# Kernel optimization log

Measured on AMD Instinct MI355X. Metric: run time of the kernel, lower is better.

The kernel has to match this reference:

```python
import jax, jax.numpy as jnp
import numpy as np

K = 3        # kernel_size
PAD = 1      # padding
STRIDE = 1   # stride (must be 1: module asserts offset HxW == input HxW)
DIL = 1      # dilation


def _bilinear_gather(x, py, px):
    """x: (B,C,H,W); py,px: (B,KK,Ho,Wo) float sample coords.
    Returns (B,C,KK,Ho,Wo), zero outside bounds (DCNv2 semantics)."""
    B, C, H, W = x.shape
    y0 = jnp.floor(py); x0 = jnp.floor(px)
    wy1 = py - y0; wy0 = 1.0 - wy1
    wx1 = px - x0; wx0 = 1.0 - wx1
    flat = x.reshape(B, C, H * W)

    def gather(yi, xi):
        valid = (yi >= 0) & (yi < H) & (xi >= 0) & (xi < W)
        yc = jnp.clip(yi, 0, H - 1).astype(jnp.int32)
        xc = jnp.clip(xi, 0, W - 1).astype(jnp.int32)
        idx = (yc * W + xc).reshape(B, 1, -1)                      # (B,1,KK*Ho*Wo)
        g = jnp.take_along_axis(flat, jnp.broadcast_to(idx, (B, C, idx.shape[-1])), axis=2)
        g = g.reshape(B, C, *yi.shape[1:])                          # (B,C,KK,Ho,Wo)
        return jnp.where(valid[:, None], g, 0.0)

    v00 = gather(y0, x0)
    v01 = gather(y0, x0 + 1)
    v10 = gather(y0 + 1, x0)
    v11 = gather(y0 + 1, x0 + 1)
    wy0 = wy0[:, None]; wy1 = wy1[:, None]; wx0 = wx0[:, None]; wx1 = wx1[:, None]
    return wy0 * (wx0 * v00 + wx1 * v01) + wy1 * (wx0 * v10 + wx1 * v11)


def dcn_v2(x, coord_offset, coord_weight, weight, bias):
    B, C, H, W = x.shape
    O = weight.shape[0]
    KK = K * K
    # offset channels ordered (k, [y,x]) per DCNv2 layout
    offs = coord_offset.reshape(B, KK, 2, H, W)
    oy, ox = offs[:, :, 0], offs[:, :, 1]
    ky, kx = jnp.meshgrid(jnp.arange(K), jnp.arange(K), indexing='ij')
    ky = ky.reshape(KK); kx = kx.reshape(KK)
    # base sampling grid for each output pixel / kernel tap: (KK,H,W)
    py = (jnp.arange(H) * STRIDE - PAD)[None, :, None] + (ky * DIL)[:, None, None]
    px = (jnp.arange(W) * STRIDE - PAD)[None, None, :] + (kx * DIL)[:, None, None]
    py = py.astype(x.dtype)[None] + oy   # (B,KK,H,W)
    px = px.astype(x.dtype)[None] + ox
    sampled = _bilinear_gather(x, py, px)              # (B,C,KK,H,W)
    sampled = sampled * coord_weight[:, None]          # modulation mask
    out = jnp.einsum('bckhw,ock->bohw', sampled, weight.reshape(O, C, KK))
    return out + bias[None, :, None, None]


def setup_inputs() -> dict:
    key = jax.random.key(0)
    k1, k2, k3, k4, k5 = jax.random.split(key, 5)
    B, C, O, H, W = 8, 256, 256, 64, 64
    return {
        'input': jax.random.normal(k1, (B, C, H, W), dtype=jnp.float32),
        'coord_offset': jax.random.normal(k2, (B, 2 * K * K, H, W), dtype=jnp.float32),
        'coord_weight': jax.random.uniform(k3, (B, K * K, H, W), dtype=jnp.float32),
        'weight': jax.random.normal(k4, (O, C, K, K), dtype=jnp.float32) * 0.02,
        'bias': jax.random.normal(k5, (O,), dtype=jnp.float32) * 0.01,
    }


def reference(input, coord_offset, coord_weight, weight, bias):
    return dcn_v2(input, coord_offset, coord_weight, weight, bias)
```

## Files before the change

kernel.cpp:

```cpp
#include <hip/hip_runtime.h>
#include <hip/hip_bf16.h>
#include <stdint.h>

typedef _Float16 f16_t;
typedef f16_t f16x8 __attribute__((ext_vector_type(8)));
typedef f16_t f16x2 __attribute__((ext_vector_type(2)));
typedef float f32x4 __attribute__((ext_vector_type(4)));

__device__ inline f16x2 as_f16x2(int v) {
    union { int i; f16x2 h; } u; u.i = v; return u.h;
}

__global__ __launch_bounds__(256) void k_prep(const float* __restrict__ x,
                                              const float* __restrict__ w,
                                              f16_t* __restrict__ xt,
                                              f16_t* __restrict__ Wp) {
    __shared__ __align__(16) char smem[36864];
    const int t = threadIdx.x;
    if (blockIdx.x < 512) {
        f16_t (*tT)[264] = (f16_t(*)[264])smem;
        const int b = blockIdx.x >> 6;
        const int y = blockIdx.x & 63;
        const float* src = x + ((size_t)(b * 256) * 64 + y) * 64;
        const int x4 = (t & 15) * 4;
        const int cs = t >> 4;
#pragma unroll
        for (int cc = 0; cc < 256; cc += 16) {
            int c = cc + cs;
            float4 v = *(const float4*)(src + (size_t)c * 4096 + x4);
            tT[x4 + 0][c] = (f16_t)v.x;
            tT[x4 + 1][c] = (f16_t)v.y;
            tT[x4 + 2][c] = (f16_t)v.z;
            tT[x4 + 3][c] = (f16_t)v.w;
        }
        __syncthreads();
        f16_t* dst = xt + ((size_t)(b * 64 + y) * 64) * 256;
#pragma unroll
        for (int i = 0; i < 8; ++i) {
            const int s = t + 256 * i;
            const int xx = s >> 5, cg = s & 31;
            *(f16x8*)(dst + xx * 256 + cg * 8) = *(const f16x8*)&tT[xx][cg * 8];
        }
    } else {
        float* lw = (float*)smem;
        const int o0 = (blockIdx.x - 512) * 4;
        const float4* src = (const float4*)(w + (size_t)o0 * 2304);
#pragma unroll
        for (int i = 0; i < 9; ++i)
            ((float4*)lw)[t + 256 * i] = src[t + 256 * i];
        __syncthreads();
#pragma unroll
        for (int i = 0; i < 5; ++i) {
            const int u = t + 256 * i;
            if (u < 1152) {
                const int o = u / 288, r = u - o * 288;
                const int kb2 = r >> 3, rr = r & 7;
                const int s = rr >> 2, qq = rr & 3;
                const int kk = kb2 >> 2, cp = kb2 & 3;
                f16x8 v;
#pragma unroll
                for (int e = 0; e < 8; ++e) {
                    const int c = cp * 64 + s * 32 + qq * 8 + e;
                    v[e] = (f16_t)lw[o * 2304 + c * 9 + kk];
                }
                *(f16x8*)(Wp + ((size_t)(kb2 * 2 + s) * 256 + o0 + o) * 32 + qq * 8) = v;
            }
        }
    }
}

__global__ __launch_bounds__(512, 4) void k_dcn(
    const f16_t* __restrict__ xt, const f16_t* __restrict__ Wp,
    const float* __restrict__ coff, const float* __restrict__ cwm,
    const float* __restrict__ bias, float* __restrict__ out) {

    __shared__ __align__(16) f16_t sS[2][64 * 64];
    __shared__ __align__(16) int2 sT[9 * 64 * 4];

    const int blk = blockIdx.x;
    const int b  = blk & 7;
    const int h  = blk >> 3;
    const int t = threadIdx.x;
    const int wv = t >> 6;
    const int lane = t & 63;

    const int p = t >> 3;
    const int q = t & 7;

    const int fr = lane & 15;
    const int quad = lane >> 4;
    const int swz = fr & 7;

    for (int u = t; u < 576; u += 512) {
        const int kk = u >> 6, wpx = u & 63;
        float oy = coff[((size_t)(b * 18 + kk * 2 + 0) * 64 + h) * 64 + wpx];
        float ox = coff[((size_t)(b * 18 + kk * 2 + 1) * 64 + h) * 64 + wpx];
        float m  = cwm [((size_t)(b * 9 + kk) * 64 + h) * 64 + wpx];
        float py = (float)(h - 1 + (kk / 3)) + oy;
        float px = (float)(wpx - 1 + (kk % 3)) + ox;
        float fy = floorf(py), fx = floorf(px);
        int y0 = (int)fy, x0 = (int)fx;
        int y1 = y0 + 1,  x1 = x0 + 1;
        float wy1 = py - fy, wx1 = px - fx;
        float wy0 = 1.0f - wy1, wx0 = 1.0f - wx1;
        bool vy0 = (y0 >= 0) && (y0 < 64), vy1 = (y1 >= 0) && (y1 < 64);
        bool vx0 = (x0 >= 0) && (x0 < 64), vx1 = (x1 >= 0) && (x1 < 64);
        int yc0 = min(max(y0, 0), 63), yc1 = min(max(y1, 0), 63);
        int xc0 = min(max(x0, 0), 63), xc1 = min(max(x1, 0), 63);
        const int base = b * 4096;
        float cw[4];
        int   ca[4];
        cw[0] = (vy0 && vx0) ? wy0 * wx0 * m : 0.0f;
        cw[1] = (vy0 && vx1) ? wy0 * wx1 * m : 0.0f;
        cw[2] = (vy1 && vx0) ? wy1 * wx0 * m : 0.0f;
        cw[3] = (vy1 && vx1) ? wy1 * wx1 * m : 0.0f;
        ca[0] = (base + yc0 * 64 + xc0) * 512;
        ca[1] = (base + yc0 * 64 + xc1) * 512;
        ca[2] = (base + yc1 * 64 + xc0) * 512;
        ca[3] = (base + yc1 * 64 + xc1) * 512;
#pragma unroll
        for (int c = 0; c < 4; ++c) {
            union { unsigned short us; f16_t hh; } cv;
            cv.hh = (f16_t)cw[c];
            int wp = (int)cv.us | ((int)cv.us << 16);
            sT[(kk * 64 + wpx) * 4 + c] = make_int2(ca[c], wp);
        }
    }
    __syncthreads();

    const f16_t* wA = Wp + (wv * 32 + fr) * 32 + quad * 8;
    f16_t* sw0 = &sS[0][p * 64 + ((q ^ (p & 7)) * 8)];
    f16_t* sw1 = sw0 + 4096;
    const int qb = q * 16;

    f32x4 acc[2][4] = {};
    f16x8 aC[2][2], aN[2][2];

    auto loadA = [&](int it, f16x8 (&a)[2][2]) {
        const f16_t* wn = wA + (size_t)it * 16384;
        a[0][0] = *(const f16x8*)(wn);
        a[0][1] = *(const f16x8*)(wn + 8192);
        a[1][0] = *(const f16x8*)(wn + 512);
        a[1][1] = *(const f16x8*)(wn + 8192 + 512);
    };

    auto do_mfma = [&](int cur) {
        const f16_t* sb = &sS[cur][0];
#pragma unroll
        for (int s = 0; s < 2; ++s) {
            const int coffe = ((s * 4 + quad) ^ swz) * 8;
            f16x8 bb[4];
#pragma unroll
            for (int nt = 0; nt < 4; ++nt)
                bb[nt] = *(const f16x8*)(sb + (nt * 16 + fr) * 64 + coffe);
#pragma unroll
            for (int mt = 0; mt < 2; ++mt)
#pragma unroll
                for (int nt = 0; nt < 4; ++nt)
                    acc[mt][nt] = __builtin_amdgcn_mfma_f32_16x16x32_f16(
                        aC[mt][s], bb[nt], acc[mt][nt], 0, 0, 0);
        }
    };

    {
        const int2* e = &sT[p * 4];
        int2 e0 = e[0], e1 = e[1], e2 = e[2], e3 = e[3];
        const char* xb = (const char*)xt;
        f16x8 g0 = *(const f16x8*)(xb + (e0.x + qb));
        f16x8 g1 = *(const f16x8*)(xb + (e1.x + qb));
        f16x8 g2 = *(const f16x8*)(xb + (e2.x + qb));
        f16x8 g3 = *(const f16x8*)(xb + (e3.x + qb));
        f16x2 w0 = as_f16x2(e0.y), w1 = as_f16x2(e1.y);
        f16x2 w2 = as_f16x2(e2.y), w3 = as_f16x2(e3.y);
        const f16x2* g0p = (const f16x2*)&g0;
        const f16x2* g1p = (const f16x2*)&g1;
        const f16x2* g2p = (const f16x2*)&g2;
        const f16x2* g3p = (const f16x2*)&g3;
        f16x8 ov; f16x2* op = (f16x2*)&ov;
#pragma unroll
        for (int j = 0; j < 4; ++j)
            op[j] = g0p[j] * w0 + g1p[j] * w1 + g2p[j] * w2 + g3p[j] * w3;
        *(f16x8*)sw0 = ov;
    }
    loadA(0, aC);
    __syncthreads();

#pragma unroll 2
    for (int it = 0; it < 36; ++it) {
        const int cur = it & 1;
        if (it < 35) {
            const int nx = it + 1;
            const int kk = nx >> 2, cp = nx & 3;
            const int2* e = &sT[(kk * 64 + p) * 4];
            int2 e0 = e[0], e1 = e[1], e2 = e[2], e3 = e[3];
            const int cb = cp * 128 + qb;
            const char* xb = (const char*)xt;
            f16x8 g0 = *(const f16x8*)(xb + (e0.x + cb));
            f16x8 g1 = *(const f16x8*)(xb + (e1.x + cb));
            f16x8 g2 = *(const f16x8*)(xb + (e2.x + cb));
            f16x8 g3 = *(const f16x8*)(xb + (e3.x + cb));
            loadA(nx, aN);
            do_mfma(cur);
            f16x2 w0 = as_f16x2(e0.y), w1 = as_f16x2(e1.y);
            f16x2 w2 = as_f16x2(e2.y), w3 = as_f16x2(e3.y);
            const f16x2* g0p = (const f16x2*)&g0;
            const f16x2* g1p = (const f16x2*)&g1;
            const f16x2* g2p = (const f16x2*)&g2;
            const f16x2* g3p = (const f16x2*)&g3;
            f16x8 ov; f16x2* op = (f16x2*)&ov;
#pragma unroll
            for (int j = 0; j < 4; ++j)
                op[j] = g0p[j] * w0 + g1p[j] * w1 + g2p[j] * w2 + g3p[j] * w3;
            *(f16x8*)(cur ? sw0 : sw1) = ov;
#pragma unroll
            for (int mt = 0; mt < 2; ++mt)
#pragma unroll
                for (int s = 0; s < 2; ++s) aC[mt][s] = aN[mt][s];
        } else {
            do_mfma(cur);
        }
        __syncthreads();
    }

    const int rowq = quad * 4;
#pragma unroll
    for (int mt = 0; mt < 2; ++mt) {
#pragma unroll
        for (int r = 0; r < 4; ++r) {
            const int og = wv * 32 + mt * 16 + rowq + r;
            const float bs = bias[og];
            float* opn = out + ((size_t)(b * 256 + og) * 64 + h) * 64;
#pragma unroll
            for (int nt = 0; nt < 4; ++nt) {
                opn[nt * 16 + fr] = acc[mt][nt][r] + bs;
            }
        }
    }
}

extern "C" void kernel_launch(void* const* d_in, const int* in_sizes, int n_in,
                              void* d_out, int out_size, void* d_ws, size_t ws_size,
                              hipStream_t stream) {
    const float* x    = (const float*)d_in[0];
    const float* coff = (const float*)d_in[1];
    const float* cwm  = (const float*)d_in[2];
    const float* wgt  = (const float*)d_in[3];
    const float* bias = (const float*)d_in[4];
    float* out = (float*)d_out;

    f16_t* xt = (f16_t*)d_ws;
    f16_t* Wp = xt + (size_t)8 * 64 * 64 * 256;

    k_prep<<<576, 256, 0, stream>>>(x, wgt, xt, Wp);
    k_dcn <<<512, 512, 0, stream>>>(xt, Wp, coff, cwm, bias, out);
}
```

Baseline: 153.3 us.

## Deepen gather prefetch to two stages, swizzle prep transpose, use lgkm-only barrier

The main loop now issues the bilinear corner gathers two iterations ahead instead of one, using parity-indexed register buffers. This gives the global loads more time to land behind the MFMA work. Sampling-table entries are read as int4 pairs, and the per-iteration __syncthreads is replaced with an inline s_waitcnt lgkmcnt(0) plus s_barrier, so the barrier no longer waits on outstanding global loads. The prep transpose in LDS switches from a padded array to an XOR-swizzled layout. The costs are more live registers, which may reduce occupancy, and reliance on hand-written barrier semantics.

```diff
diff --git a/kernel.cpp b/kernel.cpp
--- a/kernel.cpp
+++ b/kernel.cpp
@@ -10,6 +10,8 @@
 __device__ inline f16x2 as_f16x2(int v) {
     union { int i; f16x2 h; } u; u.i = v; return u.h;
 }
+
+#define LGKM_BARRIER() asm volatile("s_waitcnt lgkmcnt(0)\n\ts_barrier" ::: "memory")
 
 __global__ __launch_bounds__(256) void k_prep(const float* __restrict__ x,
                                               const float* __restrict__ w,
@@ -18,7 +20,7 @@
     __shared__ __align__(16) char smem[36864];
     const int t = threadIdx.x;
     if (blockIdx.x < 512) {
-        f16_t (*tT)[264] = (f16_t(*)[264])smem;
+        f16_t* tT = (f16_t*)smem;
         const int b = blockIdx.x >> 6;
         const int y = blockIdx.x & 63;
         const float* src = x + ((size_t)(b * 256) * 64 + y) * 64;
@@ -26,12 +28,15 @@
         const int cs = t >> 4;
 #pragma unroll
         for (int cc = 0; cc < 256; cc += 16) {
-            int c = cc + cs;
+            const int c = cc + cs;
             float4 v = *(const float4*)(src + (size_t)c * 4096 + x4);
-            tT[x4 + 0][c] = (f16_t)v.x;
-            tT[x4 + 1][c] = (f16_t)v.y;
-            tT[x4 + 2][c] = (f16_t)v.z;
-            tT[x4 + 3][c] = (f16_t)v.w;
+            const int chunk = c >> 3, e = c & 7;
+#pragma unroll
+            for (int j = 0; j < 4; ++j) {
+                const int xx = x4 + j;
+                const float f = (j == 0) ? v.x : (j == 1) ? v.y : (j == 2) ? v.z : v.w;
+                tT[xx * 256 + ((chunk ^ (xx & 31)) << 3) + e] = (f16_t)f;
+            }
         }
         __syncthreads();
         f16_t* dst = xt + ((size_t)(b * 64 + y) * 64) * 256;
@@ -39,7 +44,8 @@
         for (int i = 0; i < 8; ++i) {
             const int s = t + 256 * i;
             const int xx = s >> 5, cg = s & 31;
-            *(f16x8*)(dst + xx * 256 + cg * 8) = *(const f16x8*)&tT[xx][cg * 8];
+            *(f16x8*)(dst + xx * 256 + cg * 8) =
+                *(const f16x8*)(tT + xx * 256 + ((cg ^ (xx & 31)) << 3));
         }
     } else {
         float* lw = (float*)smem;
@@ -129,23 +135,56 @@
     __syncthreads();
 
     const f16_t* wA = Wp + (wv * 32 + fr) * 32 + quad * 8;
-    f16_t* sw0 = &sS[0][p * 64 + ((q ^ (p & 7)) * 8)];
-    f16_t* sw1 = sw0 + 4096;
+    f16_t* const swb0 = &sS[0][p * 64 + ((q ^ (p & 7)) * 8)];
     const int qb = q * 16;
 
     f32x4 acc[2][4] = {};
-    f16x8 aC[2][2], aN[2][2];
-
-    auto loadA = [&](int it, f16x8 (&a)[2][2]) {
+    f16x8 aR[2][2][2];
+    f16x8 gR[2][4];
+    int   wPk[2][4];
+
+    auto gather = [&](int it) {
+        const int par = it & 1;
+        const int kk = it >> 2, cp = it & 3;
+        const int4* tp = (const int4*)&sT[(kk * 64 + p) * 4];
+        int4 t0 = tp[0], t1 = tp[1];
+        const int cb = cp * 128 + qb;
+        const char* xb = (const char*)xt;
+        gR[par][0] = *(const f16x8*)(xb + (t0.x + cb));
+        gR[par][1] = *(const f16x8*)(xb + (t0.z + cb));
+        gR[par][2] = *(const f16x8*)(xb + (t1.x + cb));
+        gR[par][3] = *(const f16x8*)(xb + (t1.z + cb));
+        wPk[par][0] = t0.y; wPk[par][1] = t0.w;
+        wPk[par][2] = t1.y; wPk[par][3] = t1.w;
+    };
+
+    auto loadA = [&](int it) {
+        const int par = it & 1;
         const f16_t* wn = wA + (size_t)it * 16384;
-        a[0][0] = *(const f16x8*)(wn);
-        a[0][1] = *(const f16x8*)(wn + 8192);
-        a[1][0] = *(const f16x8*)(wn + 512);
-        a[1][1] = *(const f16x8*)(wn + 8192 + 512);
-    };
-
-    auto do_mfma = [&](int cur) {
-        const f16_t* sb = &sS[cur][0];
+        aR[par][0][0] = *(const f16x8*)(wn);
+        aR[par][0][1] = *(const f16x8*)(wn + 8192);
+        aR[par][1][0] = *(const f16x8*)(wn + 512);
+        aR[par][1][1] = *(const f16x8*)(wn + 8192 + 512);
+    };
+
+    auto combine = [&](int it) {
+        const int par = it & 1;
+        f16x2 w0 = as_f16x2(wPk[par][0]), w1 = as_f16x2(wPk[par][1]);
+        f16x2 w2 = as_f16x2(wPk[par][2]), w3 = as_f16x2(wPk[par][3]);
+        const f16x2* g0p = (const f16x2*)&gR[par][0];
+        const f16x2* g1p = (const f16x2*)&gR[par][1];
+        const f16x2* g2p = (const f16x2*)&gR[par][2];
+        const f16x2* g3p = (const f16x2*)&gR[par][3];
+        f16x8 ov; f16x2* op = (f16x2*)&ov;
+#pragma unroll
+        for (int j = 0; j < 4; ++j)
+            op[j] = g0p[j] * w0 + g1p[j] * w1 + g2p[j] * w2 + g3p[j] * w3;
+        *(f16x8*)(swb0 + par * 4096) = ov;
+    };
+
+    auto do_mfma = [&](int it) {
+        const int par = it & 1;
+        const f16_t* sb = &sS[par][0];
 #pragma unroll
         for (int s = 0; s < 2; ++s) {
             const int coffe = ((s * 4 + quad) ^ swz) * 8;
@@ -158,68 +197,23 @@
 #pragma unroll
                 for (int nt = 0; nt < 4; ++nt)
                     acc[mt][nt] = __builtin_amdgcn_mfma_f32_16x16x32_f16(
-                        aC[mt][s], bb[nt], acc[mt][nt], 0, 0, 0);
-        }
-    };
-
-    {
-        const int2* e = &sT[p * 4];
-        int2 e0 = e[0], e1 = e[1], e2 = e[2], e3 = e[3];
-        const char* xb = (const char*)xt;
-        f16x8 g0 = *(const f16x8*)(xb + (e0.x + qb));
-        f16x8 g1 = *(const f16x8*)(xb + (e1.x + qb));
-        f16x8 g2 = *(const f16x8*)(xb + (e2.x + qb));
-        f16x8 g3 = *(const f16x8*)(xb + (e3.x + qb));
-        f16x2 w0 = as_f16x2(e0.y), w1 = as_f16x2(e1.y);
-        f16x2 w2 = as_f16x2(e2.y), w3 = as_f16x2(e3.y);
-        const f16x2* g0p = (const f16x2*)&g0;
-        const f16x2* g1p = (const f16x2*)&g1;
-        const f16x2* g2p = (const f16x2*)&g2;
-        const f16x2* g3p = (const f16x2*)&g3;
-        f16x8 ov; f16x2* op = (f16x2*)&ov;
-#pragma unroll
-        for (int j = 0; j < 4; ++j)
-            op[j] = g0p[j] * w0 + g1p[j] * w1 + g2p[j] * w2 + g3p[j] * w3;
-        *(f16x8*)sw0 = ov;
-    }
-    loadA(0, aC);
-    __syncthreads();
+                        aR[par][mt][s], bb[nt], acc[mt][nt], 0, 0, 0);
+        }
+    };
+
+    gather(0);
+    gather(1);
+    loadA(0);
+    combine(0);
+    LGKM_BARRIER();
 
 #pragma unroll 2
     for (int it = 0; it < 36; ++it) {
-        const int cur = it & 1;
-        if (it < 35) {
-            const int nx = it + 1;
-            const int kk = nx >> 2, cp = nx & 3;
-            const int2* e = &sT[(kk * 64 + p) * 4];
-            int2 e0 = e[0], e1 = e[1], e2 = e[2], e3 = e[3];
-            const int cb = cp * 128 + qb;
-            const char* xb = (const char*)xt;
-            f16x8 g0 = *(const f16x8*)(xb + (e0.x + cb));
-            f16x8 g1 = *(const f16x8*)(xb + (e1.x + cb));
-            f16x8 g2 = *(const f16x8*)(xb + (e2.x + cb));
-            f16x8 g3 = *(const f16x8*)(xb + (e3.x + cb));
-            loadA(nx, aN);
-            do_mfma(cur);
-            f16x2 w0 = as_f16x2(e0.y), w1 = as_f16x2(e1.y);
-            f16x2 w2 = as_f16x2(e2.y), w3 = as_f16x2(e3.y);
-            const f16x2* g0p = (const f16x2*)&g0;
-            const f16x2* g1p = (const f16x2*)&g1;
-            const f16x2* g2p = (const f16x2*)&g2;
-            const f16x2* g3p = (const f16x2*)&g3;
-            f16x8 ov; f16x2* op = (f16x2*)&ov;
-#pragma unroll
-            for (int j = 0; j < 4; ++j)
-                op[j] = g0p[j] * w0 + g1p[j] * w1 + g2p[j] * w2 + g3p[j] * w3;
-            *(f16x8*)(cur ? sw0 : sw1) = ov;
-#pragma unroll
-            for (int mt = 0; mt < 2; ++mt)
-#pragma unroll
-                for (int s = 0; s < 2; ++s) aC[mt][s] = aN[mt][s];
-        } else {
-            do_mfma(cur);
-        }
-        __syncthreads();
+        if (it + 2 < 36) gather(it + 2);
+        if (it + 1 < 36) loadA(it + 1);
+        do_mfma(it);
+        if (it + 1 < 36) combine(it + 1);
+        LGKM_BARRIER();
     }
 
     const int rowq = quad * 4;
```

New measurement: 196.5 us. +28.1%, slower.

## Swizzle prep transpose LDS, vectorize table reads, use LDS-only barriers in main loop

Applied to the files above, without the earlier changes.

The prep transpose now uses an XOR-swizzled shared-memory layout in place of a padded array, to cut bank conflicts. In the main kernel, sampling-table entries are read as int4 and the bilinear blend becomes one f16x8 expression with broadcast weights. The per-iteration __syncthreads is replaced by an s_waitcnt on LDS counters plus s_barrier, so outstanding global loads no longer have to drain at every step. The sample is now finished and written to LDS before the MFMAs, which shortens the overlap between the gather loads and the matrix work.

```diff
diff --git a/kernel.cpp b/kernel.cpp
--- a/kernel.cpp
+++ b/kernel.cpp
@@ -4,11 +4,11 @@
 
 typedef _Float16 f16_t;
 typedef f16_t f16x8 __attribute__((ext_vector_type(8)));
-typedef f16_t f16x2 __attribute__((ext_vector_type(2)));
 typedef float f32x4 __attribute__((ext_vector_type(4)));
 
-__device__ inline f16x2 as_f16x2(int v) {
-    union { int i; f16x2 h; } u; u.i = v; return u.h;
+__device__ inline void lgkm_barrier() {
+    __builtin_amdgcn_s_waitcnt(0xC07F);
+    __builtin_amdgcn_s_barrier();
 }
 
 __global__ __launch_bounds__(256) void k_prep(const float* __restrict__ x,
@@ -18,7 +18,7 @@
     __shared__ __align__(16) char smem[36864];
     const int t = threadIdx.x;
     if (blockIdx.x < 512) {
-        f16_t (*tT)[264] = (f16_t(*)[264])smem;
+        f16_t* tT = (f16_t*)smem;
         const int b = blockIdx.x >> 6;
         const int y = blockIdx.x & 63;
         const float* src = x + ((size_t)(b * 256) * 64 + y) * 64;
@@ -26,12 +26,15 @@
         const int cs = t >> 4;
 #pragma unroll
         for (int cc = 0; cc < 256; cc += 16) {
-            int c = cc + cs;
+            const int c = cc + cs;
             float4 v = *(const float4*)(src + (size_t)c * 4096 + x4);
-            tT[x4 + 0][c] = (f16_t)v.x;
-            tT[x4 + 1][c] = (f16_t)v.y;
-            tT[x4 + 2][c] = (f16_t)v.z;
-            tT[x4 + 3][c] = (f16_t)v.w;
+            const int chunk = c >> 3, e = c & 7;
+#pragma unroll
+            for (int j = 0; j < 4; ++j) {
+                const int xx = x4 + j;
+                const float f = (j == 0) ? v.x : (j == 1) ? v.y : (j == 2) ? v.z : v.w;
+                tT[xx * 256 + ((chunk ^ (xx & 31)) << 3) + e] = (f16_t)f;
+            }
         }
         __syncthreads();
         f16_t* dst = xt + ((size_t)(b * 64 + y) * 64) * 256;
@@ -39,7 +42,8 @@
         for (int i = 0; i < 8; ++i) {
             const int s = t + 256 * i;
             const int xx = s >> 5, cg = s & 31;
-            *(f16x8*)(dst + xx * 256 + cg * 8) = *(const f16x8*)&tT[xx][cg * 8];
+            *(f16x8*)(dst + xx * 256 + cg * 8) =
+                *(const f16x8*)(tT + xx * 256 + ((cg ^ (xx & 31)) << 3));
         }
     } else {
         float* lw = (float*)smem;
@@ -120,17 +124,14 @@
         ca[3] = (base + yc1 * 64 + xc1) * 512;
 #pragma unroll
         for (int c = 0; c < 4; ++c) {
-            union { unsigned short us; f16_t hh; } cv;
-            cv.hh = (f16_t)cw[c];
-            int wp = (int)cv.us | ((int)cv.us << 16);
-            sT[(kk * 64 + wpx) * 4 + c] = make_int2(ca[c], wp);
+            unsigned short ws = __builtin_bit_cast(unsigned short, (f16_t)cw[c]);
+            sT[(kk * 64 + wpx) * 4 + c] = make_int2(ca[c], (int)ws);
         }
     }
     __syncthreads();
 
     const f16_t* wA = Wp + (wv * 32 + fr) * 32 + quad * 8;
-    f16_t* sw0 = &sS[0][p * 64 + ((q ^ (p & 7)) * 8)];
-    f16_t* sw1 = sw0 + 4096;
+    f16_t* const swb0 = &sS[0][p * 64 + ((q ^ (p & 7)) * 8)];
     const int qb = q * 16;
 
     f32x4 acc[2][4] = {};
@@ -162,56 +163,39 @@
         }
     };
 
-    {
-        const int2* e = &sT[p * 4];
-        int2 e0 = e[0], e1 = e[1], e2 = e[2], e3 = e[3];
+    auto sample_into = [&](int it, int buf) {
+        const int kk = it >> 2, cp = it & 3;
+        const int4* tp = (const int4*)&sT[(kk * 64 + p) * 4];
+        int4 t0 = tp[0], t1 = tp[1];
+        const int cb = cp * 128 + qb;
         const char* xb = (const char*)xt;
-        f16x8 g0 = *(const f16x8*)(xb + (e0.x + qb));
-        f16x8 g1 = *(const f16x8*)(xb + (e1.x + qb));
-        f16x8 g2 = *(const f16x8*)(xb + (e2.x + qb));
-        f16x8 g3 = *(const f16x8*)(xb + (e3.x + qb));
-        f16x2 w0 = as_f16x2(e0.y), w1 = as_f16x2(e1.y);
-        f16x2 w2 = as_f16x2(e2.y), w3 = as_f16x2(e3.y);
-        const f16x2* g0p = (const f16x2*)&g0;
-        const f16x2* g1p = (const f16x2*)&g1;
-        const f16x2* g2p = (const f16x2*)&g2;
-        const f16x2* g3p = (const f16x2*)&g3;
-        f16x8 ov; f16x2* op = (f16x2*)&ov;
-#pragma unroll
-        for (int j = 0; j < 4; ++j)
-            op[j] = g0p[j] * w0 + g1p[j] * w1 + g2p[j] * w2 + g3p[j] * w3;
-        *(f16x8*)sw0 = ov;
-    }
+        f16x8 g0 = *(const f16x8*)(xb + (t0.x + cb));
+        f16x8 g1 = *(const f16x8*)(xb + (t0.z + cb));
+        f16x8 g2 = *(const f16x8*)(xb + (t1.x + cb));
+        f16x8 g3 = *(const f16x8*)(xb + (t1.z + cb));
+        f16_t w0 = __builtin_bit_cast(f16_t, (unsigned short)t0.y);
+        f16_t w1 = __builtin_bit_cast(f16_t, (unsigned short)t0.w);
+        f16_t w2 = __builtin_bit_cast(f16_t, (unsigned short)t1.y);
+        f16_t w3 = __builtin_bit_cast(f16_t, (unsigned short)t1.w);
+        f16x8 w0v = {w0, w0, w0, w0, w0, w0, w0, w0};
+        f16x8 w1v = {w1, w1, w1, w1, w1, w1, w1, w1};
+        f16x8 w2v = {w2, w2, w2, w2, w2, w2, w2, w2};
+        f16x8 w3v = {w3, w3, w3, w3, w3, w3, w3, w3};
+        f16x8 ov = g0 * w0v + g1 * w1v + g2 * w2v + g3 * w3v;
+        *(f16x8*)(swb0 + buf * 4096) = ov;
+    };
+
+    sample_into(0, 0);
     loadA(0, aC);
-    __syncthreads();
+    lgkm_barrier();
 
 #pragma unroll 2
     for (int it = 0; it < 36; ++it) {
         const int cur = it & 1;
         if (it < 35) {
-            const int nx = it + 1;
-            const int kk = nx >> 2, cp = nx & 3;
-            const int2* e = &sT[(kk * 64 + p) * 4];
-            int2 e0 = e[0], e1 = e[1], e2 = e[2], e3 = e[3];
-            const int cb = cp * 128 + qb;
-            const char* xb = (const char*)xt;
-            f16x8 g0 = *(const f16x8*)(xb + (e0.x + cb));
-            f16x8 g1 = *(const f16x8*)(xb + (e1.x + cb));
-            f16x8 g2 = *(const f16x8*)(xb + (e2.x + cb));
-            f16x8 g3 = *(const f16x8*)(xb + (e3.x + cb));
-            loadA(nx, aN);
+            sample_into(it + 1, 1 - cur);
+            loadA(it + 1, aN);
             do_mfma(cur);
-            f16x2 w0 = as_f16x2(e0.y), w1 = as_f16x2(e1.y);
-            f16x2 w2 = as_f16x2(e2.y), w3 = as_f16x2(e3.y);
-            const f16x2* g0p = (const f16x2*)&g0;
-            const f16x2* g1p = (const f16x2*)&g1;
-            const f16x2* g2p = (const f16x2*)&g2;
-            const f16x2* g3p = (const f16x2*)&g3;
-            f16x8 ov; f16x2* op = (f16x2*)&ov;
-#pragma unroll
-            for (int j = 0; j < 4; ++j)
-                op[j] = g0p[j] * w0 + g1p[j] * w1 + g2p[j] * w2 + g3p[j] * w3;
-            *(f16x8*)(cur ? sw0 : sw1) = ov;
 #pragma unroll
             for (int mt = 0; mt < 2; ++mt)
 #pragma unroll
@@ -219,7 +203,7 @@
         } else {
             do_mfma(cur);
         }
-        __syncthreads();
+        lgkm_barrier();
     }
 
     const int rowq = quad * 4;
```

Result: faster. 149.1 us (-2.8%).
